# Kernel tuning notes

Measured on AMD Instinct MI355X. Metric: run time of the kernel, lower is better.

## Reference

```python
import jax, jax.numpy as jnp
import numpy as np

# STBLISModule forward. Original torch code materializes kron(s_wav, t_wav)
# [K*J, N*T, N*T] and contracts: filtered[b,c,d,nt] = sum_k kron[d,nt,k] x[b,c,k].
# Since kron(S_p, T_q)[n*T+t, m*T+u] = S_p[n,m] * T_q[t,u] (row-major flatten),
# this equals the separable form y[b,c,p,q] = S_p @ X[b,c] @ T_q^T, which we
# compute directly (identical math, no giant dense kron matrix).

B, C, N, T = 4, 4, 512, 256
K, J = 4, 4


def setup_inputs() -> dict:
    key = jax.random.key(0)
    k1, k2, k3 = jax.random.split(key, 3)
    x = jax.random.normal(k1, (B, C, N, T), dtype=jnp.float32)
    s_wav = jax.random.normal(k2, (K, N, N), dtype=jnp.float32)  # spatial wavelet bank
    t_wav = jax.random.normal(k3, (J, T, T), dtype=jnp.float32)  # temporal wavelet bank
    return {"x": x, "s_wav": s_wav, "t_wav": t_wav}


def reference(x, s_wav, t_wav):
    # spatial filtering: [B,C,K,N,T]
    tmp = jnp.einsum('pnm,bcmu->bcpnu', s_wav, x)
    # temporal filtering: [B,C,K,J,N,T]; note sum over last axis u of t_wav
    # matches kron/einsum 'ijk,mlk' contraction (i.e. X @ T_q^T)
    y = jnp.einsum('bcpnu,qtu->bcpqnt', tmp, t_wav)
    b, c, p, q, n, t = y.shape
    # D index ordering d = p*J + q matches torch.kron filter ordering
    y = y.reshape(b, c * p * q, n, t)
    # dual ReLU split, concatenated on channel dim
    return jnp.concatenate([jax.nn.relu(y), jax.nn.relu(-y)], axis=1)
```

## Files before the change

### kernel.cpp

```cpp
#include <hip/hip_runtime.h>
#include <hip/hip_bf16.h>

typedef __attribute__((ext_vector_type(8))) short bf16x8;
typedef __attribute__((ext_vector_type(4))) float f32x4;
typedef __attribute__((ext_vector_type(4))) int   i32x4;
typedef __attribute__((ext_vector_type(2))) int   i32x2;

#define DEV static __device__ __forceinline__

DEV unsigned short f2bf(float f) {
  __hip_bfloat16 h = __float2bfloat16(f);
  return __builtin_bit_cast(unsigned short, h);
}
DEV int pack2(float a, float b) {
  return (int)f2bf(a) | ((int)f2bf(b) << 16);
}
DEV bf16x8 ldsFrag(const char* lds, int off) {
  i32x4 v = *(const i32x4*)(lds + off);
  return __builtin_bit_cast(bf16x8, v);
}


__global__ __launch_bounds__(256) void cvt_all(
    const float* __restrict__ x, unsigned short* __restrict__ xt,
    const float* __restrict__ sw, unsigned short* __restrict__ swb,
    const float* __restrict__ tw, unsigned short* __restrict__ twb)
{
  const int bid = blockIdx.x;
  const int tid = threadIdx.x;
  if (bid < 512) {
    __shared__ unsigned short lt[64][72];
    const int ut = bid & 3;
    const int mt = (bid >> 2) & 7;
    const int bc = bid >> 5;
    const int ul = tid & 63;
    const int mr = tid >> 6;
    const float* px = x + ((size_t)bc * 512 + mt * 64) * 256 + ut * 64;
#pragma unroll
    for (int r = 0; r < 16; r++) {
      int m = r * 4 + mr;
      lt[m][ul] = f2bf(px[(size_t)m * 256 + ul]);
    }
    __syncthreads();
    const int t8 = tid >> 5;
    const int a  = t8 & 3;
    const int bb = t8 >> 2;
    const int l0 = tid & 31;
    unsigned short* tilep =
        xt + (((size_t)(bc * 16 + ut * 4 + a)) * 16 + (mt * 2 + bb)) * 512;
#pragma unroll
    for (int h = 0; h < 2; h++) {
      int l = l0 + h * 32;
      int ur = a * 16 + (l & 15);
      int mb = bb * 32 + (l >> 4) * 8;
      i32x4 w;
#pragma unroll
      for (int j = 0; j < 4; j++)
        w[j] = (int)lt[mb + 2 * j][ur] | ((int)lt[mb + 2 * j + 1][ur] << 16);
      *(i32x4*)(tilep + l * 8) = w;
    }
  } else if (bid < 1024) {
    const int tile = (bid - 512) * 4 + (tid >> 6);
    const int l = tid & 63;
    const int mt2 = tile & 15;
    const int nt2 = (tile >> 4) & 31;
    const int p   = tile >> 9;
    const float* ps = sw + ((size_t)p * 512 + nt2 * 16 + (l & 15)) * 512
                         + mt2 * 32 + (l >> 4) * 8;
    f32x4 A = ((const f32x4*)ps)[0], Bv = ((const f32x4*)ps)[1];
    i32x4 w;
    w[0] = pack2(A[0], A[1]);  w[1] = pack2(A[2], A[3]);
    w[2] = pack2(Bv[0], Bv[1]); w[3] = pack2(Bv[2], Bv[3]);
    *(i32x4*)(swb + (size_t)tile * 512 + l * 8) = w;
  } else {
    const int tile = (bid - 1024) * 4 + (tid >> 6);
    const int l = tid & 63;
    const int ut2 = tile & 7;
    const int tt2 = (tile >> 3) & 15;
    const int q   = tile >> 7;
    const float* pt = tw + ((size_t)q * 256 + tt2 * 16 + (l & 15)) * 256
                         + ut2 * 32 + (l >> 4) * 8;
    f32x4 A = ((const f32x4*)pt)[0], Bv = ((const f32x4*)pt)[1];
    i32x4 w;
    w[0] = pack2(A[0], A[1]);  w[1] = pack2(A[2], A[3]);
    w[2] = pack2(Bv[0], Bv[1]); w[3] = pack2(Bv[2], Bv[3]);
    *(i32x4*)(twb + (size_t)tile * 512 + l * 8) = w;
  }
}

__global__ __launch_bounds__(512, 4) void stblis_main(
    const unsigned short* __restrict__ xt, const unsigned short* __restrict__ swb,
    const unsigned short* __restrict__ twb, float* __restrict__ out)
{
  __shared__ __align__(16) char lds[65536];

  const int tid  = threadIdx.x;
  const int lane = tid & 63;
  const int wid  = tid >> 6;
  const int l15  = lane & 15;
  const int l4   = lane >> 4;

  const int bx = blockIdx.x;
  const int nt = bx & 7;
  const int p  = (bx >> 3) & 3;
  const int bc = bx >> 5;
  const int n0 = nt * 64;

  const int wu = wid >> 1;
  const int wn = wid & 1;

  f32x4 acc[4][2];
#pragma unroll
  for (int i = 0; i < 4; i++)
#pragma unroll
    for (int j = 0; j < 2; j++) acc[i][j] = {0.f, 0.f, 0.f, 0.f};

  const unsigned short* xA = xt  + (((size_t)(bc * 16 + wu * 4)) * 16) * 512 + lane * 8;
  const unsigned short* sB = swb + (((size_t)(p * 32 + nt * 4 + wn * 2)) * 16) * 512 + lane * 8;

  for (int kc = 0; kc < 8; kc++) {
#pragma unroll
    for (int ks = 0; ks < 2; ks++) {
      const int mt2 = kc * 2 + ks;
      bf16x8 af[4], bg[2];
#pragma unroll
      for (int uf = 0; uf < 4; uf++)
        af[uf] = *(const bf16x8*)(xA + ((size_t)uf * 16 + mt2) * 512);
#pragma unroll
      for (int nf = 0; nf < 2; nf++)
        bg[nf] = *(const bf16x8*)(sB + ((size_t)nf * 16 + mt2) * 512);
#pragma unroll
      for (int uf = 0; uf < 4; uf++)
#pragma unroll
        for (int nf = 0; nf < 2; nf++)
          acc[uf][nf] = __builtin_amdgcn_mfma_f32_16x16x32_bf16(
              af[uf], bg[nf], acc[uf][nf], 0, 0, 0);
    }
  }

#pragma unroll
  for (int uf = 0; uf < 4; uf++)
#pragma unroll
    for (int nf = 0; nf < 2; nf++) {
      int u0 = wu * 64 + uf * 16 + l4 * 4;
      int n  = wn * 32 + nf * 16 + l15;
      i32x2 w;
      w[0] = pack2(acc[uf][nf][0], acc[uf][nf][1]);
      w[1] = pack2(acc[uf][nf][2], acc[uf][nf][3]);
      *(i32x2*)(lds + n * 512 + (((u0 >> 3) ^ (n & 7)) << 4) + (u0 & 7) * 2) = w;
    }
  __syncthreads();

  const int tq = wid >> 1;
  const int nh = wid & 1;
  const int b = bc >> 2, c = bc & 3;

  for (int ph = 0; ph < 16; ph++) {
    const int q  = ph >> 2;
    const int tc = ph & 3;
    char* stgW = lds + 32768 + (ph & 1) * 16384;

    f32x4 a2[2];
    a2[0] = {0.f, 0.f, 0.f, 0.f};
    a2[1] = {0.f, 0.f, 0.f, 0.f};
    const unsigned short* tA =
        twb + (((size_t)(q * 16 + tc * 4 + tq)) * 8) * 512 + lane * 8;
#pragma unroll
    for (int us = 0; us < 8; us++) {
      bf16x8 bg = *(const bf16x8*)(tA + (size_t)us * 512);
#pragma unroll
      for (int nf = 0; nf < 2; nf++) {
        int n = nh * 32 + nf * 16 + l15;
        bf16x8 af = ldsFrag(lds, n * 512 + ((((us * 4 + l4)) ^ (n & 7)) << 4));
        a2[nf] = __builtin_amdgcn_mfma_f32_16x16x32_bf16(bg, af, a2[nf], 0, 0, 0);
      }
    }
#pragma unroll
    for (int nf = 0; nf < 2; nf++) {
      int n = nh * 32 + nf * 16 + l15;
      int c16 = tq * 4 + l4;
      *(f32x4*)(stgW + n * 256 + ((c16 ^ (n & 7)) << 4)) = a2[nf];
    }
    __syncthreads();

    float* outQP = out + ((size_t)(b * 128 + c * 16 + p * 4 + q) * 512 + n0) * 256;
    float* outQN = outQP + (size_t)64 * 512 * 256;
#pragma unroll
    for (int h = 0; h < 2; h++) {
      int cc  = tid + h * 512;
      int r   = cc >> 4;
      int o16 = cc & 15;
      f32x4 y = *(const f32x4*)(stgW + r * 256 + ((o16 ^ (r & 7)) << 4));
      f32x4 vP, vN;
#pragma unroll
      for (int j = 0; j < 4; j++) {
        vP[j] = fmaxf(y[j], 0.f);
        vN[j] = fmaxf(-y[j], 0.f);
      }
      size_t go = (size_t)r * 256 + tc * 64 + o16 * 4;
      *(f32x4*)(outQP + go) = vP;
      *(f32x4*)(outQN + go) = vN;
    }
  }
}

extern "C" void kernel_launch(void* const* d_in, const int* in_sizes, int n_in,
                              void* d_out, int out_size, void* d_ws, size_t ws_size,
                              hipStream_t stream) {
  (void)in_sizes; (void)n_in; (void)out_size; (void)ws_size;
  const float* x  = (const float*)d_in[0];
  const float* sw = (const float*)d_in[1];
  const float* tw = (const float*)d_in[2];
  float* out = (float*)d_out;

  unsigned short* xt  = (unsigned short*)d_ws;
  unsigned short* swb = xt + (size_t)16 * 16 * 16 * 512;
  unsigned short* twb = swb + (size_t)2048 * 512;

  cvt_all<<<dim3(1152), dim3(256), 0, stream>>>(x, xt, sw, swb, tw, twb);
  stblis_main<<<dim3(512), dim3(512), 0, stream>>>(xt, swb, twb, out);
}
```

Before: 71.87 us.

## Cache LDS fragments in registers and double-buffer temporal weight prefetch

The spatial-stage result fragments are loaded from LDS into registers once, instead of being re-read in each of the 16 temporal phases. That frees the LDS, which is then reused for output staging, halving the shared allocation to 32KB. Temporal wavelet fragments for the next phase are prefetched from global memory into a second register set while the current phase runs. This adds a large number of live VGPRs under a tight launch-bounds occupancy target, so register spilling is possible, and the kernel is likely dominated by output write bandwidth anyway.

```diff
diff --git a/kernel.cpp b/kernel.cpp
--- a/kernel.cpp
+++ b/kernel.cpp
@@ -92,7 +92,7 @@
     const unsigned short* __restrict__ xt, const unsigned short* __restrict__ swb,
     const unsigned short* __restrict__ twb, float* __restrict__ out)
 {
-  __shared__ __align__(16) char lds[65536];
+  __shared__ __align__(16) char lds[32768];
 
   const int tid  = threadIdx.x;
   const int lane = tid & 63;
@@ -105,6 +105,7 @@
   const int p  = (bx >> 3) & 3;
   const int bc = bx >> 5;
   const int n0 = nt * 64;
+  const int b = bc >> 2, c = bc & 3;
 
   const int wu = wid >> 1;
   const int wn = wid & 1;
@@ -153,27 +154,43 @@
 
   const int tq = wid >> 1;
   const int nh = wid & 1;
-  const int b = bc >> 2, c = bc & 3;
-
-  for (int ph = 0; ph < 16; ph++) {
+
+#define LOADBG(dst, ph)                                                        \
+  {                                                                            \
+    const int q_ = (ph) >> 2, tc_ = (ph) & 3;                                  \
+    const unsigned short* tA_ =                                                \
+        twb + (((size_t)(q_ * 16 + tc_ * 4 + tq)) * 8) * 512 + lane * 8;       \
+    _Pragma("unroll")                                                          \
+    for (int us = 0; us < 8; us++)                                             \
+      dst[us] = *(const bf16x8*)(tA_ + (size_t)us * 512);                      \
+  }
+
+  bf16x8 bgA[8], bgB[8];
+  LOADBG(bgA, 0);
+
+  bf16x8 afr[8][2];
+#pragma unroll
+  for (int us = 0; us < 8; us++)
+#pragma unroll
+    for (int nf = 0; nf < 2; nf++) {
+      int n = nh * 32 + nf * 16 + l15;
+      afr[us][nf] = ldsFrag(lds, n * 512 + (((us * 4 + l4) ^ (n & 7)) << 4));
+    }
+  __syncthreads();
+
+  char* const stg0 = lds;
+  char* const stg1 = lds + 16384;
+
+  auto body = [&](int ph, bf16x8 (&bg)[8], char* stgW) {
     const int q  = ph >> 2;
     const int tc = ph & 3;
-    char* stgW = lds + 32768 + (ph & 1) * 16384;
-
     f32x4 a2[2];
     a2[0] = {0.f, 0.f, 0.f, 0.f};
     a2[1] = {0.f, 0.f, 0.f, 0.f};
-    const unsigned short* tA =
-        twb + (((size_t)(q * 16 + tc * 4 + tq)) * 8) * 512 + lane * 8;
 #pragma unroll
     for (int us = 0; us < 8; us++) {
-      bf16x8 bg = *(const bf16x8*)(tA + (size_t)us * 512);
-#pragma unroll
-      for (int nf = 0; nf < 2; nf++) {
-        int n = nh * 32 + nf * 16 + l15;
-        bf16x8 af = ldsFrag(lds, n * 512 + ((((us * 4 + l4)) ^ (n & 7)) << 4));
-        a2[nf] = __builtin_amdgcn_mfma_f32_16x16x32_bf16(bg, af, a2[nf], 0, 0, 0);
-      }
+      a2[0] = __builtin_amdgcn_mfma_f32_16x16x32_bf16(bg[us], afr[us][0], a2[0], 0, 0, 0);
+      a2[1] = __builtin_amdgcn_mfma_f32_16x16x32_bf16(bg[us], afr[us][1], a2[1], 0, 0, 0);
     }
 #pragma unroll
     for (int nf = 0; nf < 2; nf++) {
@@ -182,7 +199,6 @@
       *(f32x4*)(stgW + n * 256 + ((c16 ^ (n & 7)) << 4)) = a2[nf];
     }
     __syncthreads();
-
     float* outQP = out + ((size_t)(b * 128 + c * 16 + p * 4 + q) * 512 + n0) * 256;
     float* outQN = outQP + (size_t)64 * 512 * 256;
 #pragma unroll
@@ -201,7 +217,16 @@
       *(f32x4*)(outQP + go) = vP;
       *(f32x4*)(outQN + go) = vN;
     }
-  }
+  };
+
+  for (int ph2 = 0; ph2 < 8; ph2++) {
+    const int ph = ph2 * 2;
+    LOADBG(bgB, ph + 1);
+    body(ph, bgA, stg0);
+    if (ph2 < 7) LOADBG(bgA, ph + 2);
+    body(ph + 1, bgB, stg1);
+  }
+#undef LOADBG
 }
 
 extern "C" void kernel_launch(void* const* d_in, const int* in_sizes, int n_in,
```

Result: faster. 70.19 us (median of 2 runs) (-2.3%).

## Software-pipeline temporal-wavelet loads and widen output phases to 128 columns

Applied to the files above, without the earlier changes.

Restructures the second GEMM stage. It processes two 64-column chunks per phase (8 phases instead of 16), staging 128-column outputs in a single 32KB buffer with a 16-way XOR swizzle. The global loads of the temporal wavelet fragments are software-pipelined into register double buffers (bgA/bgB), so they overlap with MFMAs and LDS reads. It also halves the number of barriers, using raw s_barrier asm in place of __syncthreads, and writes wider contiguous output rows. The cost is more VGPR pressure from the 16 held fragments, which could affect occupancy at launch_bounds(512,4), and the hand-written barriers need careful ordering to stay correct.

```diff
diff --git a/kernel.cpp b/kernel.cpp
--- a/kernel.cpp
+++ b/kernel.cpp
@@ -15,8 +15,8 @@
 DEV int pack2(float a, float b) {
   return (int)f2bf(a) | ((int)f2bf(b) << 16);
 }
-DEV bf16x8 ldsFrag(const char* lds, int off) {
-  i32x4 v = *(const i32x4*)(lds + off);
+DEV bf16x8 ldsFrag(const char* p, int off) {
+  i32x4 v = *(const i32x4*)(p + off);
   return __builtin_bit_cast(bf16x8, v);
 }
 
@@ -93,6 +93,8 @@
     const unsigned short* __restrict__ twb, float* __restrict__ out)
 {
   __shared__ __align__(16) char lds[65536];
+  char* const tmp = lds;
+  char* const stg = lds + 32768;
 
   const int tid  = threadIdx.x;
   const int lane = tid & 63;
@@ -105,6 +107,7 @@
   const int p  = (bx >> 3) & 3;
   const int bc = bx >> 5;
   const int n0 = nt * 64;
+  const int b = bc >> 2, c = bc & 3;
 
   const int wu = wid >> 1;
   const int wn = wid & 1;
@@ -147,61 +150,80 @@
       i32x2 w;
       w[0] = pack2(acc[uf][nf][0], acc[uf][nf][1]);
       w[1] = pack2(acc[uf][nf][2], acc[uf][nf][3]);
-      *(i32x2*)(lds + n * 512 + (((u0 >> 3) ^ (n & 7)) << 4) + (u0 & 7) * 2) = w;
+      *(i32x2*)(tmp + n * 512 + (((u0 >> 3) ^ (n & 7)) << 4) + (u0 & 7) * 2) = w;
     }
   __syncthreads();
 
   const int tq = wid >> 1;
   const int nh = wid & 1;
-  const int b = bc >> 2, c = bc & 3;
-
-  for (int ph = 0; ph < 16; ph++) {
-    const int q  = ph >> 2;
-    const int tc = ph & 3;
-    char* stgW = lds + 32768 + (ph & 1) * 16384;
-
-    f32x4 a2[2];
-    a2[0] = {0.f, 0.f, 0.f, 0.f};
-    a2[1] = {0.f, 0.f, 0.f, 0.f};
-    const unsigned short* tA =
-        twb + (((size_t)(q * 16 + tc * 4 + tq)) * 8) * 512 + lane * 8;
-#pragma unroll
-    for (int us = 0; us < 8; us++) {
-      bf16x8 bg = *(const bf16x8*)(tA + (size_t)us * 512);
-#pragma unroll
-      for (int nf = 0; nf < 2; nf++) {
-        int n = nh * 32 + nf * 16 + l15;
-        bf16x8 af = ldsFrag(lds, n * 512 + ((((us * 4 + l4)) ^ (n & 7)) << 4));
-        a2[nf] = __builtin_amdgcn_mfma_f32_16x16x32_bf16(bg, af, a2[nf], 0, 0, 0);
-      }
-    }
-#pragma unroll
-    for (int nf = 0; nf < 2; nf++) {
-      int n = nh * 32 + nf * 16 + l15;
-      int c16 = tq * 4 + l4;
-      *(f32x4*)(stgW + n * 256 + ((c16 ^ (n & 7)) << 4)) = a2[nf];
-    }
-    __syncthreads();
+  const int rowA = nh * 32 + l15;
+  const int rowB = nh * 32 + 16 + l15;
+
+  bf16x8 bgA[8], bgB[8];
+
+#define LOADBG(dst, ph16)                                                      \
+  {                                                                            \
+    const int q_ = (ph16) >> 2, tc_ = (ph16) & 3;                              \
+    const unsigned short* tA_ =                                                \
+        twb + (((size_t)(q_ * 16 + tc_ * 4 + tq)) * 8) * 512 + lane * 8;       \
+    _Pragma("unroll")                                                          \
+    for (int us_ = 0; us_ < 8; us_++)                                          \
+      dst[us_] = *(const bf16x8*)(tA_ + (size_t)us_ * 512);                    \
+  }
+
+#define SUB(cur, tcl)                                                          \
+  {                                                                            \
+    f32x4 a20 = {0.f, 0.f, 0.f, 0.f};                                          \
+    f32x4 a21 = {0.f, 0.f, 0.f, 0.f};                                          \
+    _Pragma("unroll")                                                          \
+    for (int us_ = 0; us_ < 8; us_++) {                                        \
+      const int slot_ = (us_ * 4 + l4) ^ (l15 & 7);                            \
+      bf16x8 af0_ = ldsFrag(tmp, rowA * 512 + (slot_ << 4));                   \
+      bf16x8 af1_ = ldsFrag(tmp, rowB * 512 + (slot_ << 4));                   \
+      a20 = __builtin_amdgcn_mfma_f32_16x16x32_bf16(cur[us_], af0_, a20, 0, 0, 0); \
+      a21 = __builtin_amdgcn_mfma_f32_16x16x32_bf16(cur[us_], af1_, a21, 0, 0, 0); \
+    }                                                                          \
+    const int c32_ = (tcl) * 16 + tq * 4 + l4;                                 \
+    *(f32x4*)(stg + rowA * 512 + ((c32_ ^ (rowA & 15)) << 4)) = a20;           \
+    *(f32x4*)(stg + rowB * 512 + ((c32_ ^ (rowB & 15)) << 4)) = a21;           \
+  }
+
+  LOADBG(bgA, 0);
+
+  for (int ph = 0; ph < 8; ph++) {
+    const int q  = ph >> 1;
+    const int th = ph & 1;
+
+    if (ph) asm volatile("s_barrier" ::: "memory");
+
+    LOADBG(bgB, 2 * ph + 1);
+    SUB(bgA, 0);
+    if (ph < 7) LOADBG(bgA, 2 * ph + 2);
+    SUB(bgB, 1);
+
+    asm volatile("s_waitcnt lgkmcnt(0)\n\ts_barrier" ::: "memory");
 
     float* outQP = out + ((size_t)(b * 128 + c * 16 + p * 4 + q) * 512 + n0) * 256;
     float* outQN = outQP + (size_t)64 * 512 * 256;
 #pragma unroll
-    for (int h = 0; h < 2; h++) {
-      int cc  = tid + h * 512;
-      int r   = cc >> 4;
-      int o16 = cc & 15;
-      f32x4 y = *(const f32x4*)(stgW + r * 256 + ((o16 ^ (r & 7)) << 4));
+    for (int it = 0; it < 4; it++) {
+      int g   = it * 512 + tid;
+      int r   = g >> 5;
+      int c32 = g & 31;
+      f32x4 y = *(const f32x4*)(stg + r * 512 + ((c32 ^ (r & 15)) << 4));
       f32x4 vP, vN;
 #pragma unroll
       for (int j = 0; j < 4; j++) {
         vP[j] = fmaxf(y[j], 0.f);
         vN[j] = fmaxf(-y[j], 0.f);
       }
-      size_t go = (size_t)r * 256 + tc * 64 + o16 * 4;
+      size_t go = (size_t)r * 256 + th * 128 + c32 * 4;
       *(f32x4*)(outQP + go) = vP;
       *(f32x4*)(outQN + go) = vN;
     }
   }
+#undef SUB
+#undef LOADBG
 }
 
 extern "C" void kernel_launch(void* const* d_in, const int* in_sizes, int n_in,
```

Result: slower. 74.17 us (+3.2%).
